# Optimization experiments

Measured on AMD Instinct MI355X. Metric: run time of the kernel, lower is better.

## Reference

```python
import jax, jax.numpy as jnp
import numpy as np

N, F, T, H = 1024, 22, 1000, 64
EPS = 1e-5


def setup_inputs() -> dict:
    key = jax.random.key(0)
    ks = iter(jax.random.split(key, 64))
    def rn(shape, s=0.1):
        return jax.random.normal(next(ks), shape, jnp.float32) * s
    inp = {"x": rn((N, F, T), 1.0)}
    in_dims = [F, H, H]
    for l in range(3):
        inp[f"Wih{l}"] = rn((4 * H, in_dims[l]))
        inp[f"Whh{l}"] = rn((4 * H, H))
        inp[f"bih{l}"] = rn((4 * H,))
        inp[f"bhh{l}"] = rn((4 * H,))
    fc = [(64, 54), (54, 44), (44, 24), (24, 4)]
    for i, (di, do) in enumerate(fc):
        inp[f"w{i}"] = rn((do, di))
        inp[f"b{i}"] = rn((do,))
    for i, d in enumerate([54, 44, 24]):
        inp[f"g{i}"] = jnp.ones((d,), jnp.float32)
        inp[f"be{i}"] = jnp.zeros((d,), jnp.float32)
        inp[f"m{i}"] = rn((d,))
        inp[f"v{i}"] = jax.random.uniform(next(ks), (d,), jnp.float32) + 0.5
    return inp


def _lstm_layer(xs, Wih, Whh, b):
    # xs: (T, N, in) -> hs: (T, N, H)
    n = xs.shape[1]
    h0 = jnp.zeros((n, Whh.shape[1]), xs.dtype)
    def step(carry, xt):
        h, c = carry
        z = xt @ Wih.T + h @ Whh.T + b  # (N, 4H)
        i, f, g, o = jnp.split(z, 4, axis=-1)  # PyTorch gate order i,f,g,o
        c = jax.nn.sigmoid(f) * c + jax.nn.sigmoid(i) * jnp.tanh(g)
        h = jax.nn.sigmoid(o) * jnp.tanh(c)
        return (h, c), h
    (_, _), hs = jax.lax.scan(step, (h0, h0), xs)
    return hs


def _bn(x, g, be, m, v):
    return (x - m) * jax.lax.rsqrt(v + EPS) * g + be


def reference(x, Wih0, Whh0, bih0, bhh0, Wih1, Whh1, bih1, bhh1,
              Wih2, Whh2, bih2, bhh2,
              w0, b0, g0, be0, m0, v0,
              w1, b1, g1, be1, m1, v1,
              w2, b2, g2, be2, m2, v2,
              w3, b3):
    # (N, F, T) -> permute(0,2,1) -> (N, T, F); scan over time-major (T, N, F)
    xs = jnp.transpose(x, (2, 0, 1))
    xs = _lstm_layer(xs, Wih0, Whh0, bih0 + bhh0)
    xs = _lstm_layer(xs, Wih1, Whh1, bih1 + bhh1)
    xs = _lstm_layer(xs, Wih2, Whh2, bih2 + bhh2)
    h = xs[-1]  # last timestep, (N, H)
    h = jax.nn.relu(_bn(h @ w0.T + b0, g0, be0, m0, v0))
    h = jax.nn.relu(_bn(h @ w1.T + b1, g1, be1, m1, v1))
    h = jax.nn.relu(_bn(h @ w2.T + b2, g2, be2, m2, v2))
    return h @ w3.T + b3
```

## Files before the change

kernel.cpp:

```cpp
#include <hip/hip_runtime.h>
#include <hip/hip_fp16.h>

#define TT 1000
#define FF 22
#define HH 64
#define BB 4
#define NBLK 256
#define S0 112
#define S1 144
#define SL0 (4 * S0)
#define SL1 (4 * S1)

typedef _Float16 half8 __attribute__((ext_vector_type(8)));
typedef float float4v __attribute__((ext_vector_type(4)));

__device__ __forceinline__ float sel4(const float4v a, int q) {
    float lo = (q & 2) ? a[2] : a[0];
    float hi = (q & 2) ? a[3] : a[1];
    return (q & 1) ? hi : lo;
}

__device__ __forceinline__ float gate_fused(const float z[4], float& c) {
    float e0 = __expf(-z[0]);
    float e1 = __expf(-z[1]);
    float e2 = __expf(2.0f * z[2]);
    float d1 = 1.0f + e1;
    float d2 = (1.0f + e0) * (1.0f + e2);
    float r  = __builtin_amdgcn_rcpf(d1 * d2);
    float f  = d2 * r;
    float ig = (e2 - 1.0f) * (d1 * r);
    float cc = __builtin_fmaf(f, c, ig);
    c = cc;
    float e3 = __expf(-z[3]);
    float e4 = __expf(2.0f * cc);
    float r2 = __builtin_amdgcn_rcpf((1.0f + e3) * (1.0f + e4));
    return (e4 - 1.0f) * r2;
}

#define LFENCE() asm volatile("s_waitcnt lgkmcnt(0)" ::: "memory")
#define BAR()    __builtin_amdgcn_s_barrier()

extern "C" __global__ void __launch_bounds__(896, 1)
lstm_fused(const float* __restrict__ x,
           const float* __restrict__ Wih0, const float* __restrict__ Whh0,
           const float* __restrict__ bih0, const float* __restrict__ bhh0,
           const float* __restrict__ Wih1, const float* __restrict__ Whh1,
           const float* __restrict__ bih1, const float* __restrict__ bhh1,
           const float* __restrict__ Wih2, const float* __restrict__ Whh2,
           const float* __restrict__ bih2, const float* __restrict__ bhh2,
           const float* __restrict__ w0, const float* __restrict__ b0,
           const float* __restrict__ w1, const float* __restrict__ b1,
           const float* __restrict__ w2, const float* __restrict__ b2,
           const float* __restrict__ w3, const float* __restrict__ b3,
           const float* __restrict__ g0, const float* __restrict__ be0,
           const float* __restrict__ m0, const float* __restrict__ v0,
           const float* __restrict__ g1, const float* __restrict__ be1,
           const float* __restrict__ m1, const float* __restrict__ v1,
           const float* __restrict__ g2, const float* __restrict__ be2,
           const float* __restrict__ m2, const float* __restrict__ v2,
           float* __restrict__ out)
{
    __shared__ __align__(16) _Float16 in0[8 * SL0];
    __shared__ __align__(16) _Float16 in1[8 * SL1];
    __shared__ __align__(16) _Float16 in2[8 * SL1];
    __shared__ float fcA[BB * 64];
    __shared__ float fcB[BB * 64];
    __shared__ float fcW[54 * 65];
    __shared__ float fcP[5 * 64];

    const int tid  = threadIdx.x;
    const int wv   = tid >> 6;
    const int role = wv >> 2;
    const int w4   = wv & 3;
    const int l    = tid & 63;
    const int q    = l >> 4;
    const int l15  = l & 15;
    const int u    = 16 * w4 + l15;
    const int b    = q;
    const int n0   = blockIdx.x * BB;

    for (int i = tid; i < 8 * SL0; i += 896) in0[i] = (_Float16)0.0f;
    for (int i = tid; i < 8 * SL1; i += 896) in1[i] = (_Float16)0.0f;
    for (int i = tid; i < 8 * SL1; i += 896) in2[i] = (_Float16)0.0f;

    half8 wf[4][4];
    float4v biasC[4];
    if (role == 2) {
#pragma unroll
        for (int g = 0; g < 4; ++g) {
            const int row = 64 * g + u;
#pragma unroll
            for (int kt = 0; kt < 3; ++kt) {
                half8 h{};
#pragma unroll
                for (int j = 0; j < 8; ++j) {
                    const int k = 32 * kt + 8 * q + j;
                    float val = 0.0f;
                    if (k < 32) { if (k < FF) val = Wih0[row * FF + k]; }
                    else        { val = Whh0[row * HH + (k - 32)]; }
                    h[j] = (_Float16)val;
                }
                wf[g][kt] = h;
            }
            float bv = bih0[row] + bhh0[row];
            biasC[g] = float4v{bv, bv, bv, bv};
        }
    } else if (role < 2) {
        const float* Wih = role ? Wih1 : Wih2;
        const float* Whh = role ? Whh1 : Whh2;
        const float* bih = role ? bih1 : bih2;
        const float* bhh = role ? bhh1 : bhh2;
#pragma unroll
        for (int g = 0; g < 4; ++g) {
            const int row = 64 * g + u;
#pragma unroll
            for (int kt = 0; kt < 4; ++kt) {
                half8 h{};
#pragma unroll
                for (int j = 0; j < 8; ++j) {
                    const int k = 32 * kt + 8 * q + j;
                    h[j] = (_Float16)((k < 64) ? Wih[row * HH + k] : Whh[row * HH + (k - 64)]);
                }
                wf[g][kt] = h;
            }
            float bv = bih[row] + bhh[row];
            biasC[g] = float4v{bv, bv, bv, bv};
        }
    }

    const int  st  = tid - 768;
    const bool xok = (role == 3) && (st >= 0) && (st < BB * FF);
    const int  xb  = xok ? (st / FF) : 0;
    const int  xf  = xok ? (st - xb * FF) : 0;
    const float* xp = x + ((size_t)(n0 + xb) * FF + xf) * TT;

    __syncthreads();

    if (xok) in0[0 * SL0 + xb * S0 + xf] = (_Float16)xp[0];
    float xA = xok ? xp[1] : 0.f;
    float xB = xok ? xp[2] : 0.f;

    const int arow = (role == 2) ? ((l15 & 3) * S0 + q * 8) : ((l15 & 3) * S1 + q * 8);
    float c = 0.f;

    if (role == 2)      __builtin_amdgcn_s_setprio(3);
    else if (role == 1) __builtin_amdgcn_s_setprio(2);
    else if (role == 0) __builtin_amdgcn_s_setprio(1);

    for (int k = 0; k < 126; ++k) {
#pragma unroll
        for (int s = 0; s < 8; ++s) {
            const int tau = 8 * k + s;
            LFENCE();
            BAR();

            if (role == 3) {
                if (tau <= TT - 2) {
                    if (xok) in0[((s + 1) & 7) * SL0 + xb * S0 + xf] = (_Float16)xA;
                    xA = xB;
                    if (xok) {
                        int tn = tau + 3; if (tn > TT - 1) tn = TT - 1;
                        xB = xp[tn];
                    }
                }
            } else if (role == 2) {
                if (tau <= TT - 1) {
                    const _Float16* rd = in0 + s * SL0;
                    half8 a0 = *(const half8*)(rd + arow);
                    half8 a1 = *(const half8*)(rd + arow + 32);
                    half8 a2 = *(const half8*)(rd + arow + 64);
                    float4v acc[4];
#pragma unroll
                    for (int g = 0; g < 4; ++g)
                        acc[g] = __builtin_amdgcn_mfma_f32_16x16x32_f16(a0, wf[g][0], biasC[g], 0, 0, 0);
#pragma unroll
                    for (int g = 0; g < 4; ++g)
                        acc[g] = __builtin_amdgcn_mfma_f32_16x16x32_f16(a1, wf[g][1], acc[g], 0, 0, 0);
#pragma unroll
                    for (int g = 0; g < 4; ++g)
                        acc[g] = __builtin_amdgcn_mfma_f32_16x16x32_f16(a2, wf[g][2], acc[g], 0, 0, 0);
                    float z[4];
#pragma unroll
                    for (int g = 0; g < 4; ++g) z[g] = sel4(acc[g], q);
                    float h = gate_fused(z, c);
                    _Float16 hf = (_Float16)h;
                    in0[((s + 1) & 7) * SL0 + b * S0 + 32 + u] = hf;
                    in1[s * SL1 + b * S1 + u]                  = hf;
                }
            } else if (role == 1) {
                if (tau >= 1 && tau <= TT) {
                    const int sr = (s + 7) & 7;
                    const _Float16* rd = in1 + sr * SL1;
                    half8 a0 = *(const half8*)(rd + arow);
                    half8 a1 = *(const half8*)(rd + arow + 32);
                    half8 a2 = *(const half8*)(rd + arow + 64);
                    half8 a3 = *(const half8*)(rd + arow + 96);
                    float4v acc[4];
#pragma unroll
                    for (int g = 0; g < 4; ++g)
                        acc[g] = __builtin_amdgcn_mfma_f32_16x16x32_f16(a0, wf[g][0], biasC[g], 0, 0, 0);
#pragma unroll
                    for (int g = 0; g < 4; ++g)
                        acc[g] = __builtin_amdgcn_mfma_f32_16x16x32_f16(a1, wf[g][1], acc[g], 0, 0, 0);
#pragma unroll
                    for (int g = 0; g < 4; ++g)
                        acc[g] = __builtin_amdgcn_mfma_f32_16x16x32_f16(a2, wf[g][2], acc[g], 0, 0, 0);
#pragma unroll
                    for (int g = 0; g < 4; ++g)
                        acc[g] = __builtin_amdgcn_mfma_f32_16x16x32_f16(a3, wf[g][3], acc[g], 0, 0, 0);
                    float z[4];
#pragma unroll
                    for (int g = 0; g < 4; ++g) z[g] = sel4(acc[g], q);
                    float h = gate_fused(z, c);
                    _Float16 hf = (_Float16)h;
                    in1[s * SL1 + b * S1 + 64 + u] = hf;
                    in2[sr * SL1 + b * S1 + u]     = hf;
                }
            } else {
                if (tau >= 2 && tau <= TT + 1) {
                    const int sr = (s + 6) & 7;
                    const _Float16* rd = in2 + sr * SL1;
                    half8 a0 = *(const half8*)(rd + arow);
                    half8 a1 = *(const half8*)(rd + arow + 32);
                    half8 a2 = *(const half8*)(rd + arow + 64);
                    half8 a3 = *(const half8*)(rd + arow + 96);
                    float4v acc[4];
#pragma unroll
                    for (int g = 0; g < 4; ++g)
                        acc[g] = __builtin_amdgcn_mfma_f32_16x16x32_f16(a0, wf[g][0], biasC[g], 0, 0, 0);
#pragma unroll
                    for (int g = 0; g < 4; ++g)
                        acc[g] = __builtin_amdgcn_mfma_f32_16x16x32_f16(a1, wf[g][1], acc[g], 0, 0, 0);
#pragma unroll
                    for (int g = 0; g < 4; ++g)
                        acc[g] = __builtin_amdgcn_mfma_f32_16x16x32_f16(a2, wf[g][2], acc[g], 0, 0, 0);
#pragma unroll
                    for (int g = 0; g < 4; ++g)
                        acc[g] = __builtin_amdgcn_mfma_f32_16x16x32_f16(a3, wf[g][3], acc[g], 0, 0, 0);
                    float z[4];
#pragma unroll
                    for (int g = 0; g < 4; ++g) z[g] = sel4(acc[g], q);
                    float h = gate_fused(z, c);
                    if (tau != TT + 1) {
                        in2[((s + 7) & 7) * SL1 + b * S1 + 64 + u] = (_Float16)h;
                    } else {
                        fcA[b * 64 + u] = h;
                    }
                }
            }
        }
    }

    __builtin_amdgcn_s_setprio(0);
    __syncthreads();

    for (int i = tid; i < 54 * 64; i += 896) fcW[(i >> 6) * 65 + (i & 63)] = w0[i];
    for (int i = tid; i < 54; i += 896) {
        fcP[i] = b0[i]; fcP[64 + i] = g0[i]; fcP[128 + i] = be0[i];
        fcP[192 + i] = m0[i]; fcP[256 + i] = v0[i];
    }
    __syncthreads();
    for (int idx = tid; idx < BB * 54; idx += 896) {
        const int bb = idx / 54, j = idx - bb * 54;
        float s = fcP[j];
        for (int k = 0; k < 64; ++k) s += fcW[j * 65 + k] * fcA[bb * 64 + k];
        s = (s - fcP[192 + j]) * rsqrtf(fcP[256 + j] + 1e-5f) * fcP[64 + j] + fcP[128 + j];
        fcB[bb * 64 + j] = fmaxf(s, 0.0f);
    }
    __syncthreads();

    for (int i = tid; i < 44 * 54; i += 896) fcW[(i / 54) * 55 + (i % 54)] = w1[i];
    for (int i = tid; i < 44; i += 896) {
        fcP[i] = b1[i]; fcP[64 + i] = g1[i]; fcP[128 + i] = be1[i];
        fcP[192 + i] = m1[i]; fcP[256 + i] = v1[i];
    }
    __syncthreads();
    for (int idx = tid; idx < BB * 44; idx += 896) {
        const int bb = idx / 44, j = idx - bb * 44;
        float s = fcP[j];
        for (int k = 0; k < 54; ++k) s += fcW[j * 55 + k] * fcB[bb * 64 + k];
        s = (s - fcP[192 + j]) * rsqrtf(fcP[256 + j] + 1e-5f) * fcP[64 + j] + fcP[128 + j];
        fcA[bb * 64 + j] = fmaxf(s, 0.0f);
    }
    __syncthreads();

    for (int i = tid; i < 24 * 44; i += 896) fcW[(i / 44) * 45 + (i % 44)] = w2[i];
    for (int i = tid; i < 24; i += 896) {
        fcP[i] = b2[i]; fcP[64 + i] = g2[i]; fcP[128 + i] = be2[i];
        fcP[192 + i] = m2[i]; fcP[256 + i] = v2[i];
    }
    __syncthreads();
    for (int idx = tid; idx < BB * 24; idx += 896) {
        const int bb = idx / 24, j = idx - bb * 24;
        float s = fcP[j];
        for (int k = 0; k < 44; ++k) s += fcW[j * 45 + k] * fcA[bb * 64 + k];
        s = (s - fcP[192 + j]) * rsqrtf(fcP[256 + j] + 1e-5f) * fcP[64 + j] + fcP[128 + j];
        fcB[bb * 64 + j] = fmaxf(s, 0.0f);
    }
    __syncthreads();

    for (int i = tid; i < 4 * 24; i += 896) fcW[(i / 24) * 25 + (i % 24)] = w3[i];
    for (int i = tid; i < 4; i += 896) fcP[i] = b3[i];
    __syncthreads();
    for (int idx = tid; idx < BB * 4; idx += 896) {
        const int bb = idx / 4, j = idx - bb * 4;
        float s = fcP[j];
        for (int k = 0; k < 24; ++k) s += fcW[j * 25 + k] * fcB[bb * 64 + k];
        out[(size_t)(n0 + bb) * 4 + j] = s;
    }
}

extern "C" void kernel_launch(void* const* d_in, const int* in_sizes, int n_in,
                              void* d_out, int out_size, void* d_ws, size_t ws_size,
                              hipStream_t stream) {
    const float* p[33];
    for (int i = 0; i < 33; ++i) p[i] = (const float*)d_in[i];
    lstm_fused<<<NBLK, 896, 0, stream>>>(
        p[0],
        p[1], p[2], p[3], p[4],
        p[5], p[6], p[7], p[8],
        p[9], p[10], p[11], p[12],
        p[13], p[14], p[15], p[16], p[17], p[18], p[19], p[20],
        p[21], p[22], p[23], p[24],
        p[25], p[26], p[27], p[28],
        p[29], p[30], p[31], p[32],
        (float*)d_out);
}
```

Measured before the change: 779.8 us.

## Split each LSTM wavefront step into two barrier phases to overlap MFMA and gates

Each time step is split into two barrier-separated phases. Layers 0 and 1 compute gate nonlinearities in phase one and their MFMA matmuls in phase two, while layer 2 does the reverse, so MFMA work of one layer overlaps the transcendental work of another. Accumulators are now carried across the phase boundary, the pipeline skew grows by one step, and the per-role wave priorities are removed. The cost is twice as many block barriers per step, and the gain depends on whether the phases balance better than the old single-phase critical path.

After: 946.2 us. +21.3%, slower.

```diff
diff --git a/kernel.cpp b/kernel.cpp
--- a/kernel.cpp
+++ b/kernel.cpp
@@ -37,8 +37,9 @@
     return (e4 - 1.0f) * r2;
 }
 
-#define LFENCE() asm volatile("s_waitcnt lgkmcnt(0)" ::: "memory")
-#define BAR()    __builtin_amdgcn_s_barrier()
+#define SYNC() do { asm volatile("s_waitcnt lgkmcnt(0)" ::: "memory"); \
+                    __builtin_amdgcn_s_barrier(); \
+                    asm volatile("" ::: "memory"); } while (0)
 
 extern "C" __global__ void __launch_bounds__(896, 1)
 lstm_fused(const float* __restrict__ x,
@@ -136,40 +137,77 @@
 
     __syncthreads();
 
-    if (xok) in0[0 * SL0 + xb * S0 + xf] = (_Float16)xp[0];
-    float xA = xok ? xp[1] : 0.f;
-    float xB = xok ? xp[2] : 0.f;
+    float xA = xok ? xp[0] : 0.f;
+    float xB = xok ? xp[1] : 0.f;
 
     const int arow = (role == 2) ? ((l15 & 3) * S0 + q * 8) : ((l15 & 3) * S1 + q * 8);
     float c = 0.f;
-
-    if (role == 2)      __builtin_amdgcn_s_setprio(3);
-    else if (role == 1) __builtin_amdgcn_s_setprio(2);
-    else if (role == 0) __builtin_amdgcn_s_setprio(1);
+    float4v acc[4] = {};
 
     for (int k = 0; k < 126; ++k) {
 #pragma unroll
         for (int s = 0; s < 8; ++s) {
-            const int tau = 8 * k + s;
-            LFENCE();
-            BAR();
-
+            const int n = 8 * k + s;
+
+            SYNC();
             if (role == 3) {
-                if (tau <= TT - 2) {
-                    if (xok) in0[((s + 1) & 7) * SL0 + xb * S0 + xf] = (_Float16)xA;
+                if (n <= TT - 1) {
+                    if (xok) in0[s * SL0 + xb * S0 + xf] = (_Float16)xA;
                     xA = xB;
                     if (xok) {
-                        int tn = tau + 3; if (tn > TT - 1) tn = TT - 1;
+                        int tn = n + 2; if (tn > TT - 1) tn = TT - 1;
                         xB = xp[tn];
                     }
                 }
             } else if (role == 2) {
-                if (tau <= TT - 1) {
+                if (n >= 1 && n <= TT) {
+                    float z[4];
+#pragma unroll
+                    for (int g = 0; g < 4; ++g) z[g] = sel4(acc[g], q);
+                    float h = gate_fused(z, c);
+                    _Float16 hf = (_Float16)h;
+                    in0[s * SL0 + b * S0 + 32 + u]          = hf;
+                    in1[((s + 7) & 7) * SL1 + b * S1 + u]   = hf;
+                }
+            } else if (role == 1) {
+                if (n >= 2 && n <= TT + 1) {
+                    float z[4];
+#pragma unroll
+                    for (int g = 0; g < 4; ++g) z[g] = sel4(acc[g], q);
+                    float h = gate_fused(z, c);
+                    _Float16 hf = (_Float16)h;
+                    in1[((s + 7) & 7) * SL1 + b * S1 + 64 + u] = hf;
+                    in2[((s + 6) & 7) * SL1 + b * S1 + u]      = hf;
+                }
+            } else {
+                if (n >= 3 && n <= TT + 2) {
+                    const _Float16* rd = in2 + ((s + 5) & 7) * SL1;
+                    half8 a0 = *(const half8*)(rd + arow);
+                    half8 a1 = *(const half8*)(rd + arow + 32);
+                    half8 a2 = *(const half8*)(rd + arow + 64);
+                    half8 a3 = *(const half8*)(rd + arow + 96);
+#pragma unroll
+                    for (int g = 0; g < 4; ++g)
+                        acc[g] = __builtin_amdgcn_mfma_f32_16x16x32_f16(a0, wf[g][0], biasC[g], 0, 0, 0);
+#pragma unroll
+                    for (int g = 0; g < 4; ++g)
+                        acc[g] = __builtin_amdgcn_mfma_f32_16x16x32_f16(a1, wf[g][1], acc[g], 0, 0, 0);
+#pragma unroll
+                    for (int g = 0; g < 4; ++g)
+                        acc[g] = __builtin_amdgcn_mfma_f32_16x16x32_f16(a2, wf[g][2], acc[g], 0, 0, 0);
+#pragma unroll
+                    for (int g = 0; g < 4; ++g)
+                        acc[g] = __builtin_amdgcn_mfma_f32_16x16x32_f16(a3, wf[g][3], acc[g], 0, 0, 0);
+                }
+            }
+
+            SYNC();
+            if (role == 2) {
+                if (n <= TT - 1) {
                     const _Float16* rd = in0 + s * SL0;
                     half8 a0 = *(const half8*)(rd + arow);
                     half8 a1 = *(const half8*)(rd + arow + 32);
                     half8 a2 = *(const half8*)(rd + arow + 64);
-                    float4v acc[4];
 #pragma unroll
                     for (int g = 0; g < 4; ++g)
                         acc[g] = __builtin_amdgcn_mfma_f32_16x16x32_f16(a0, wf[g][0], biasC[g], 0, 0, 0);
@@ -179,23 +217,14 @@
 #pragma unroll
                     for (int g = 0; g < 4; ++g)
                         acc[g] = __builtin_amdgcn_mfma_f32_16x16x32_f16(a2, wf[g][2], acc[g], 0, 0, 0);
-                    float z[4];
-#pragma unroll
-                    for (int g = 0; g < 4; ++g) z[g] = sel4(acc[g], q);
-                    float h = gate_fused(z, c);
-                    _Float16 hf = (_Float16)h;
-                    in0[((s + 1) & 7) * SL0 + b * S0 + 32 + u] = hf;
-                    in1[s * SL1 + b * S1 + u]                  = hf;
                 }
             } else if (role == 1) {
-                if (tau >= 1 && tau <= TT) {
-                    const int sr = (s + 7) & 7;
-                    const _Float16* rd = in1 + sr * SL1;
+                if (n >= 1 && n <= TT) {
+                    const _Float16* rd = in1 + ((s + 7) & 7) * SL1;
                     half8 a0 = *(const half8*)(rd + arow);
                     half8 a1 = *(const half8*)(rd + arow + 32);
                     half8 a2 = *(const half8*)(rd + arow + 64);
                     half8 a3 = *(const half8*)(rd + arow + 96);
-                    float4v acc[4];
 #pragma unroll
                     for (int g = 0; g < 4; ++g)
                         acc[g] = __builtin_amdgcn_mfma_f32_16x16x32_f16(a0, wf[g][0], biasC[g], 0, 0, 0);
@@ -208,41 +237,15 @@
 #pragma unroll
                     for (int g = 0; g < 4; ++g)
                         acc[g] = __builtin_amdgcn_mfma_f32_16x16x32_f16(a3, wf[g][3], acc[g], 0, 0, 0);
+                }
+            } else if (role == 0) {
+                if (n >= 3 && n <= TT + 2) {
                     float z[4];
 #pragma unroll
                     for (int g = 0; g < 4; ++g) z[g] = sel4(acc[g], q);
                     float h = gate_fused(z, c);
-                    _Float16 hf = (_Float16)h;
-                    in1[s * SL1 + b * S1 + 64 + u] = hf;
-                    in2[sr * SL1 + b * S1 + u]     = hf;
-                }
-            } else {
-                if (tau >= 2 && tau <= TT + 1) {
-                    const int sr = (s + 6) & 7;
-                    const _Float16* rd = in2 + sr * SL1;
-                    half8 a0 = *(const half8*)(rd + arow);
-                    half8 a1 = *(const half8*)(rd + arow + 32);
-                    half8 a2 = *(const half8*)(rd + arow + 64);
-                    half8 a3 = *(const half8*)(rd + arow + 96);
-                    float4v acc[4];
-#pragma unroll
-                    for (int g = 0; g < 4; ++g)
-                        acc[g] = __builtin_amdgcn_mfma_f32_16x16x32_f16(a0, wf[g][0], biasC[g], 0, 0, 0);
-#pragma unroll
-                    for (int g = 0; g < 4; ++g)
-                        acc[g] = __builtin_amdgcn_mfma_f32_16x16x32_f16(a1, wf[g][1], acc[g], 0, 0, 0);
-#pragma unroll
-                    for (int g = 0; g < 4; ++g)
-                        acc[g] = __builtin_amdgcn_mfma_f32_16x16x32_f16(a2, wf[g][2], acc[g], 0, 0, 0);
-#pragma unroll
-                    for (int g = 0; g < 4; ++g)
-                        acc[g] = __builtin_amdgcn_mfma_f32_16x16x32_f16(a3, wf[g][3], acc[g], 0, 0, 0);
-                    float z[4];
-#pragma unroll
-                    for (int g = 0; g < 4; ++g) z[g] = sel4(acc[g], q);
-                    float h = gate_fused(z, c);
-                    if (tau != TT + 1) {
-                        in2[((s + 7) & 7) * SL1 + b * S1 + 64 + u] = (_Float16)h;
+                    if (n != TT + 2) {
+                        in2[((s + 6) & 7) * SL1 + b * S1 + 64 + u] = (_Float16)h;
                     } else {
                         fcA[b * 64 + u] = h;
                     }
@@ -251,7 +254,6 @@
         }
     }
 
-    __builtin_amdgcn_s_setprio(0);
     __syncthreads();
 
     for (int i = tid; i < 54 * 64; i += 896) fcW[(i >> 6) * 65 + (i & 63)] = w0[i];
```

## Merge layer-1 and layer-2 LSTM waves and fold x-loading into layer-0 waves

Applied to the files above, without the earlier changes.

Warp roles are restructured from 14 waves (3 layer groups plus an x-loader group) to 8 waves. Four 'heavy' waves compute both layer 1 and layer 2 each step, and four waves handle layer 0 together with x prefetch. Block size drops from 896 to 512 with launch bounds allowing 2 blocks per CU, and biases are now added after the MFMA rather than used as its initial accumulator. This cuts per-barrier wave count and allows more resident blocks, but it doubles the serial MFMA and gate work per heavy wave and raises register pressure from holding two weight sets.

Result: slower. 1.064 ms (+36.5%).

```diff
diff --git a/kernel.cpp b/kernel.cpp
--- a/kernel.cpp
+++ b/kernel.cpp
@@ -37,10 +37,11 @@
     return (e4 - 1.0f) * r2;
 }
 
-#define LFENCE() asm volatile("s_waitcnt lgkmcnt(0)" ::: "memory")
-#define BAR()    __builtin_amdgcn_s_barrier()
-
-extern "C" __global__ void __launch_bounds__(896, 1)
+#define SYNC() do { asm volatile("s_waitcnt lgkmcnt(0)" ::: "memory"); \
+                    __builtin_amdgcn_s_barrier(); \
+                    asm volatile("" ::: "memory"); } while (0)
+
+extern "C" __global__ void __launch_bounds__(512, 2)
 lstm_fused(const float* __restrict__ x,
            const float* __restrict__ Wih0, const float* __restrict__ Whh0,
            const float* __restrict__ bih0, const float* __restrict__ bhh0,
@@ -68,24 +69,44 @@
     __shared__ float fcW[54 * 65];
     __shared__ float fcP[5 * 64];
 
-    const int tid  = threadIdx.x;
-    const int wv   = tid >> 6;
-    const int role = wv >> 2;
-    const int w4   = wv & 3;
-    const int l    = tid & 63;
-    const int q    = l >> 4;
-    const int l15  = l & 15;
-    const int u    = 16 * w4 + l15;
-    const int b    = q;
-    const int n0   = blockIdx.x * BB;
-
-    for (int i = tid; i < 8 * SL0; i += 896) in0[i] = (_Float16)0.0f;
-    for (int i = tid; i < 8 * SL1; i += 896) in1[i] = (_Float16)0.0f;
-    for (int i = tid; i < 8 * SL1; i += 896) in2[i] = (_Float16)0.0f;
-
-    half8 wf[4][4];
-    float4v biasC[4];
-    if (role == 2) {
+    const int tid   = threadIdx.x;
+    const int wv    = tid >> 6;
+    const bool heavy = (wv < 4);
+    const int cset  = heavy ? wv : (wv - 4);
+    const int l     = tid & 63;
+    const int q     = l >> 4;
+    const int l15   = l & 15;
+    const int u     = 16 * cset + l15;
+    const int b     = q;
+    const int n0    = blockIdx.x * BB;
+
+    for (int i = tid; i < 8 * SL0; i += 512) in0[i] = (_Float16)0.0f;
+    for (int i = tid; i < 8 * SL1; i += 512) in1[i] = (_Float16)0.0f;
+    for (int i = tid; i < 8 * SL1; i += 512) in2[i] = (_Float16)0.0f;
+
+    half8 wf1[4][4], wf2[4][4];
+    half8 wf0[4][3];
+    float bv1[4], bv2[4], bv0[4];
+    if (heavy) {
+#pragma unroll
+        for (int g = 0; g < 4; ++g) {
+            const int row = 64 * g + u;
+#pragma unroll
+            for (int kt = 0; kt < 4; ++kt) {
+                half8 h{}, h2{};
+#pragma unroll
+                for (int j = 0; j < 8; ++j) {
+                    const int k = 32 * kt + 8 * q + j;
+                    h[j]  = (_Float16)((k < 64) ? Wih1[row * HH + k] : Whh1[row * HH + (k - 64)]);
+                    h2[j] = (_Float16)((k < 64) ? Wih2[row * HH + k] : Whh2[row * HH + (k - 64)]);
+                }
+                wf1[g][kt] = h;
+                wf2[g][kt] = h2;
+            }
+            bv1[g] = bih1[row] + bhh1[row];
+            bv2[g] = bih2[row] + bhh2[row];
+        }
+    } else {
 #pragma unroll
         for (int g = 0; g < 4; ++g) {
             const int row = 64 * g + u;
@@ -100,167 +121,139 @@
                     else        { val = Whh0[row * HH + (k - 32)]; }
                     h[j] = (_Float16)val;
                 }
-                wf[g][kt] = h;
+                wf0[g][kt] = h;
             }
-            float bv = bih0[row] + bhh0[row];
-            biasC[g] = float4v{bv, bv, bv, bv};
+            bv0[g] = bih0[row] + bhh0[row];
         }
-    } else if (role < 2) {
-        const float* Wih = role ? Wih1 : Wih2;
-        const float* Whh = role ? Whh1 : Whh2;
-        const float* bih = role ? bih1 : bih2;
-        const float* bhh = role ? bhh1 : bhh2;
-#pragma unroll
-        for (int g = 0; g < 4; ++g) {
-            const int row = 64 * g + u;
-#pragma unroll
-            for (int kt = 0; kt < 4; ++kt) {
-                half8 h{};
-#pragma unroll
-                for (int j = 0; j < 8; ++j) {
-                    const int k = 32 * kt + 8 * q + j;
-                    h[j] = (_Float16)((k < 64) ? Wih[row * HH + k] : Whh[row * HH + (k - 64)]);
-                }
-                wf[g][kt] = h;
-            }
-            float bv = bih[row] + bhh[row];
-            biasC[g] = float4v{bv, bv, bv, bv};
-        }
-    }
-
-    const int  st  = tid - 768;
-    const bool xok = (role == 3) && (st >= 0) && (st < BB * FF);
-    const int  xb  = xok ? (st / FF) : 0;
-    const int  xf  = xok ? (st - xb * FF) : 0;
-    const float* xp = x + ((size_t)(n0 + xb) * FF + xf) * TT;
-
-    __syncthreads();
-
-    if (xok) in0[0 * SL0 + xb * S0 + xf] = (_Float16)xp[0];
+    }
+
+    const bool xok = (!heavy) && (l < FF);
+    const int  xb  = cset;
+    const float* xp = x + ((size_t)(n0 + xb) * FF + l) * TT;
+
+    __syncthreads();
+
+    if (xok) in0[0 * SL0 + xb * S0 + l] = (_Float16)xp[0];
     float xA = xok ? xp[1] : 0.f;
     float xB = xok ? xp[2] : 0.f;
 
-    const int arow = (role == 2) ? ((l15 & 3) * S0 + q * 8) : ((l15 & 3) * S1 + q * 8);
-    float c = 0.f;
-
-    if (role == 2)      __builtin_amdgcn_s_setprio(3);
-    else if (role == 1) __builtin_amdgcn_s_setprio(2);
-    else if (role == 0) __builtin_amdgcn_s_setprio(1);
+    const int arow = heavy ? ((l15 & 3) * S1 + q * 8) : ((l15 & 3) * S0 + q * 8);
+    float c1 = 0.f, c2 = 0.f, c0 = 0.f;
+    const float4v zz = {0.f, 0.f, 0.f, 0.f};
 
     for (int k = 0; k < 126; ++k) {
 #pragma unroll
         for (int s = 0; s < 8; ++s) {
             const int tau = 8 * k + s;
-            LFENCE();
-            BAR();
-
-            if (role == 3) {
+            SYNC();
+
+            if (heavy) {
+                const bool do1 = (tau >= 1) && (tau <= TT);
+                const bool do2 = (tau >= 2) && (tau <= TT + 1);
+                float4v A1[4], A2[4];
+                if (do1) {
+                    const _Float16* rd = in1 + ((s + 7) & 7) * SL1;
+                    half8 a0 = *(const half8*)(rd + arow);
+                    half8 a1 = *(const half8*)(rd + arow + 32);
+                    half8 a2 = *(const half8*)(rd + arow + 64);
+                    half8 a3 = *(const half8*)(rd + arow + 96);
+#pragma unroll
+                    for (int g = 0; g < 4; ++g)
+                        A1[g] = __builtin_amdgcn_mfma_f32_16x16x32_f16(a0, wf1[g][0], zz, 0, 0, 0);
+#pragma unroll
+                    for (int g = 0; g < 4; ++g)
+                        A1[g] = __builtin_amdgcn_mfma_f32_16x16x32_f16(a1, wf1[g][1], A1[g], 0, 0, 0);
+#pragma unroll
+                    for (int g = 0; g < 4; ++g)
+                        A1[g] = __builtin_amdgcn_mfma_f32_16x16x32_f16(a2, wf1[g][2], A1[g], 0, 0, 0);
+#pragma unroll
+                    for (int g = 0; g < 4; ++g)
+                        A1[g] = __builtin_amdgcn_mfma_f32_16x16x32_f16(a3, wf1[g][3], A1[g], 0, 0, 0);
+                }
+                if (do2) {
+                    const _Float16* rd = in2 + ((s + 6) & 7) * SL1;
+                    half8 a0 = *(const half8*)(rd + arow);
+                    half8 a1 = *(const half8*)(rd + arow + 32);
+                    half8 a2 = *(const half8*)(rd + arow + 64);
+                    half8 a3 = *(const half8*)(rd + arow + 96);
+#pragma unroll
+                    for (int g = 0; g < 4; ++g)
+                        A2[g] = __builtin_amdgcn_mfma_f32_16x16x32_f16(a0, wf2[g][0], zz, 0, 0, 0);
+#pragma unroll
+                    for (int g = 0; g < 4; ++g)
+                        A2[g] = __builtin_amdgcn_mfma_f32_16x16x32_f16(a1, wf2[g][1], A2[g], 0, 0, 0);
+#pragma unroll
+                    for (int g = 0; g < 4; ++g)
+                        A2[g] = __builtin_amdgcn_mfma_f32_16x16x32_f16(a2, wf2[g][2], A2[g], 0, 0, 0);
+#pragma unroll
+                    for (int g = 0; g < 4; ++g)
+                        A2[g] = __builtin_amdgcn_mfma_f32_16x16x32_f16(a3, wf2[g][3], A2[g], 0, 0, 0);
+                }
+                if (do1) {
+                    float z[4];
+#pragma unroll
+                    for (int g = 0; g < 4; ++g) z[g] = sel4(A1[g], q) + bv1[g];
+                    float h = gate_fused(z, c1);
+                    _Float16 hf = (_Float16)h;
+                    in1[s * SL1 + b * S1 + 64 + u]            = hf;
+                    in2[((s + 7) & 7) * SL1 + b * S1 + u]     = hf;
+                }
+                if (do2) {
+                    float z[4];
+#pragma unroll
+                    for (int g = 0; g < 4; ++g) z[g] = sel4(A2[g], q) + bv2[g];
+                    float h = gate_fused(z, c2);
+                    if (tau != TT + 1) {
+                        in2[((s + 7) & 7) * SL1 + b * S1 + 64 + u] = (_Float16)h;
+                    } else {
+                        fcA[b * 64 + u] = h;
+                    }
+                }
+            } else {
                 if (tau <= TT - 2) {
-                    if (xok) in0[((s + 1) & 7) * SL0 + xb * S0 + xf] = (_Float16)xA;
+                    if (xok) in0[((s + 1) & 7) * SL0 + xb * S0 + l] = (_Float16)xA;
                     xA = xB;
                     if (xok) {
                         int tn = tau + 3; if (tn > TT - 1) tn = TT - 1;
                         xB = xp[tn];
                     }
                 }
-            } else if (role == 2) {
                 if (tau <= TT - 1) {
                     const _Float16* rd = in0 + s * SL0;
                     half8 a0 = *(const half8*)(rd + arow);
                     half8 a1 = *(const half8*)(rd + arow + 32);
                     half8 a2 = *(const half8*)(rd + arow + 64);
-                    float4v acc[4];
-#pragma unroll
-                    for (int g = 0; g < 4; ++g)
-                        acc[g] = __builtin_amdgcn_mfma_f32_16x16x32_f16(a0, wf[g][0], biasC[g], 0, 0, 0);
-#pragma unroll
-                    for (int g = 0; g < 4; ++g)
-                        acc[g] = __builtin_amdgcn_mfma_f32_16x16x32_f16(a1, wf[g][1], acc[g], 0, 0, 0);
-#pragma unroll
-                    for (int g = 0; g < 4; ++g)
-                        acc[g] = __builtin_amdgcn_mfma_f32_16x16x32_f16(a2, wf[g][2], acc[g], 0, 0, 0);
+                    float4v A0[4];
+#pragma unroll
+                    for (int g = 0; g < 4; ++g)
+                        A0[g] = __builtin_amdgcn_mfma_f32_16x16x32_f16(a0, wf0[g][0], zz, 0, 0, 0);
+#pragma unroll
+                    for (int g = 0; g < 4; ++g)
+                        A0[g] = __builtin_amdgcn_mfma_f32_16x16x32_f16(a1, wf0[g][1], A0[g], 0, 0, 0);
+#pragma unroll
+                    for (int g = 0; g < 4; ++g)
+                        A0[g] = __builtin_amdgcn_mfma_f32_16x16x32_f16(a2, wf0[g][2], A0[g], 0, 0, 0);
                     float z[4];
 #pragma unroll
-                    for (int g = 0; g < 4; ++g) z[g] = sel4(acc[g], q);
-                    float h = gate_fused(z, c);
+                    for (int g = 0; g < 4; ++g) z[g] = sel4(A0[g], q) + bv0[g];
+                    float h = gate_fused(z, c0);
                     _Float16 hf = (_Float16)h;
                     in0[((s + 1) & 7) * SL0 + b * S0 + 32 + u] = hf;
                     in1[s * SL1 + b * S1 + u]                  = hf;
                 }
-            } else if (role == 1) {
-                if (tau >= 1 && tau <= TT) {
-                    const int sr = (s + 7) & 7;
-                    const _Float16* rd = in1 + sr * SL1;
-                    half8 a0 = *(const half8*)(rd + arow);
-                    half8 a1 = *(const half8*)(rd + arow + 32);
-                    half8 a2 = *(const half8*)(rd + arow + 64);
-                    half8 a3 = *(const half8*)(rd + arow + 96);
-                    float4v acc[4];
-#pragma unroll
-                    for (int g = 0; g < 4; ++g)
-                        acc[g] = __builtin_amdgcn_mfma_f32_16x16x32_f16(a0, wf[g][0], biasC[g], 0, 0, 0);
-#pragma unroll
-                    for (int g = 0; g < 4; ++g)
-                        acc[g] = __builtin_amdgcn_mfma_f32_16x16x32_f16(a1, wf[g][1], acc[g], 0, 0, 0);
-#pragma unroll
-                    for (int g = 0; g < 4; ++g)
-                        acc[g] = __builtin_amdgcn_mfma_f32_16x16x32_f16(a2, wf[g][2], acc[g], 0, 0, 0);
-#pragma unroll
-                    for (int g = 0; g < 4; ++g)
-                        acc[g] = __builtin_amdgcn_mfma_f32_16x16x32_f16(a3, wf[g][3], acc[g], 0, 0, 0);
-                    float z[4];
-#pragma unroll
-                    for (int g = 0; g < 4; ++g) z[g] = sel4(acc[g], q);
-                    float h = gate_fused(z, c);
-                    _Float16 hf = (_Float16)h;
-                    in1[s * SL1 + b * S1 + 64 + u] = hf;
-                    in2[sr * SL1 + b * S1 + u]     = hf;
-                }
-            } else {
-                if (tau >= 2 && tau <= TT + 1) {
-                    const int sr = (s + 6) & 7;
-                    const _Float16* rd = in2 + sr * SL1;
-                    half8 a0 = *(const half8*)(rd + arow);
-                    half8 a1 = *(const half8*)(rd + arow + 32);
-                    half8 a2 = *(const half8*)(rd + arow + 64);
-                    half8 a3 = *(const half8*)(rd + arow + 96);
-                    float4v acc[4];
-#pragma unroll
-                    for (int g = 0; g < 4; ++g)
-                        acc[g] = __builtin_amdgcn_mfma_f32_16x16x32_f16(a0, wf[g][0], biasC[g], 0, 0, 0);
-#pragma unroll
-                    for (int g = 0; g < 4; ++g)
-                        acc[g] = __builtin_amdgcn_mfma_f32_16x16x32_f16(a1, wf[g][1], acc[g], 0, 0, 0);
-#pragma unroll
-                    for (int g = 0; g < 4; ++g)
-                        acc[g] = __builtin_amdgcn_mfma_f32_16x16x32_f16(a2, wf[g][2], acc[g], 0, 0, 0);
-#pragma unroll
-                    for (int g = 0; g < 4; ++g)
-                        acc[g] = __builtin_amdgcn_mfma_f32_16x16x32_f16(a3, wf[g][3], acc[g], 0, 0, 0);
-                    float z[4];
-#pragma unroll
-                    for (int g = 0; g < 4; ++g) z[g] = sel4(acc[g], q);
-                    float h = gate_fused(z, c);
-                    if (tau != TT + 1) {
-                        in2[((s + 7) & 7) * SL1 + b * S1 + 64 + u] = (_Float16)h;
-                    } else {
-                        fcA[b * 64 + u] = h;
-                    }
-                }
             }
         }
     }
 
-    __builtin_amdgcn_s_setprio(0);
-    __syncthreads();
-
-    for (int i = tid; i < 54 * 64; i += 896) fcW[(i >> 6) * 65 + (i & 63)] = w0[i];
-    for (int i = tid; i < 54; i += 896) {
+    __syncthreads();
+
+    for (int i = tid; i < 54 * 64; i += 512) fcW[(i >> 6) * 65 + (i & 63)] = w0[i];
+    for (int i = tid; i < 54; i += 512) {
         fcP[i] = b0[i]; fcP[64 + i] = g0[i]; fcP[128 + i] = be0[i];
         fcP[192 + i] = m0[i]; fcP[256 + i] = v0[i];
     }
     __syncthreads();
-    for (int idx = tid; idx < BB * 54; idx += 896) {
+    for (int idx = tid; idx < BB * 54; idx += 512) {
         const int bb = idx / 54, j = idx - bb * 54;
         float s = fcP[j];
         for (int k = 0; k < 64; ++k) s += fcW[j * 65 + k] * fcA[bb * 64 + k];
@@ -269,13 +262,13 @@
     }
     __syncthreads();
 
-    for (int i = tid; i < 44 * 54; i += 896) fcW[(i / 54) * 55 + (i % 54)] = w1[i];
-    for (int i = tid; i < 44; i += 896) {
+    for (int i = tid; i < 44 * 54; i += 512) fcW[(i / 54) * 55 + (i % 54)] = w1[i];
+    for (int i = tid; i < 44; i += 512) {
         fcP[i] = b1[i]; fcP[64 + i] = g1[i]; fcP[128 + i] = be1[i];
         fcP[192 + i] = m1[i]; fcP[256 + i] = v1[i];
     }
     __syncthreads();
-    for (int idx = tid; idx < BB * 44; idx += 896) {
+    for (int idx = tid; idx < BB * 44; idx += 512) {
         const int bb = idx / 44, j = idx - bb * 44;
         float s = fcP[j];
         for (int k = 0; k < 54; ++k) s += fcW[j * 55 + k] * fcB[bb * 64 + k];
@@ -284,13 +277,13 @@
     }
     __syncthreads();
 
-    for (int i = tid; i < 24 * 44; i += 896) fcW[(i / 44) * 45 + (i % 44)] = w2[i];
-    for (int i = tid; i < 24; i += 896) {
+    for (int i = tid; i < 24 * 44; i += 512) fcW[(i / 44) * 45 + (i % 44)] = w2[i];
+    for (int i = tid; i < 24; i += 512) {
         fcP[i] = b2[i]; fcP[64 + i] = g2[i]; fcP[128 + i] = be2[i];
         fcP[192 + i] = m2[i]; fcP[256 + i] = v2[i];
     }
     __syncthreads();
-    for (int idx = tid; idx < BB * 24; idx += 896) {
+    for (int idx = tid; idx < BB * 24; idx += 512) {
         const int bb = idx / 24, j = idx - bb * 24;
         float s = fcP[j];
         for (int k = 0; k < 44; ++k) s += fcW[j * 45 + k] * fcA[bb * 64 + k];
@@ -299,10 +292,10 @@
     }
     __syncthreads();
 
-    for (int i = tid; i < 4 * 24; i += 896) fcW[(i / 24) * 25 + (i % 24)] = w3[i];
-    for (int i = tid; i < 4; i += 896) fcP[i] = b3[i];
-    __syncthreads();
-    for (int idx = tid; idx < BB * 4; idx += 896) {
+    for (int i = tid; i < 4 * 24; i += 512) fcW[(i / 24) * 25 + (i % 24)] = w3[i];
+    for (int i = tid; i < 4; i += 512) fcP[i] = b3[i];
+    __syncthreads();
+    for (int idx = tid; idx < BB * 4; idx += 512) {
         const int bb = idx / 4, j = idx - bb * 4;
         float s = fcP[j];
         for (int k = 0; k < 24; ++k) s += fcW[j * 25 + k] * fcB[bb * 64 + k];
@@ -315,7 +308,7 @@
                               hipStream_t stream) {
     const float* p[33];
     for (int i = 0; i < 33; ++i) p[i] = (const float*)d_in[i];
-    lstm_fused<<<NBLK, 896, 0, stream>>>(
+    lstm_fused<<<NBLK, 512, 0, stream>>>(
         p[0],
         p[1], p[2], p[3], p[4],
         p[5], p[6], p[7], p[8],
```
